# Optimization experiments

Hardware: AMD Instinct MI355X
Metric: run time of the kernel (lower is better)

## Reference

```python
import jax, jax.numpy as jnp
import numpy as np

DIM = 1024
NUM_HEADS = 16
HEAD_DIM = DIM // NUM_HEADS
SCALE = 1.0 / float(np.sqrt(HEAD_DIM))


def setup_inputs() -> dict:
    key = jax.random.key(0)
    ks = jax.random.split(key, 5)
    B, S = 2, 2048
    x = jax.random.normal(ks[0], (B, S, DIM), dtype=jnp.float32)
    qkv_w = jax.random.normal(ks[1], (3 * DIM, DIM), dtype=jnp.float32) * (1.0 / np.sqrt(DIM))
    qkv_b = jax.random.normal(ks[2], (3 * DIM,), dtype=jnp.float32) * 0.02
    proj_w = jax.random.normal(ks[3], (DIM, DIM), dtype=jnp.float32) * (1.0 / np.sqrt(DIM))
    proj_b = jax.random.normal(ks[4], (DIM,), dtype=jnp.float32) * 0.02
    return {"x": x, "qkv_w": qkv_w, "qkv_b": qkv_b, "proj_w": proj_w, "proj_b": proj_b}


def reference(x, qkv_w, qkv_b, proj_w, proj_b):
    B, S, _ = x.shape
    # qkv projection: (B,S,3*DIM) -> (3, B, H, S, Dh)
    qkv = x @ qkv_w.T + qkv_b
    qkv = qkv.reshape(B, S, 3, NUM_HEADS, HEAD_DIM).transpose(2, 0, 3, 1, 4)
    q, k, v = qkv[0], qkv[1], qkv[2]
    # scaled dot-product attention (full score matrix, as in the original)
    scores = jnp.einsum('bhqd,bhkd->bhqk', q, k) * SCALE
    attn = jax.nn.softmax(scores, axis=-1)
    out = jnp.einsum('bhqk,bhkd->bhqd', attn, v)  # (B,H,S,Dh)
    out = out.transpose(0, 2, 1, 3).reshape(B, S, DIM)
    return out @ proj_w.T + proj_b
```

## Files before the change

### kernel.cpp

```cpp
#include <hip/hip_runtime.h>

#define DIM_ 1024
#define NH_ 16
#define HD_ 64
#define B_ 2
#define S_ 2048
#define M_ (B_ * S_)
#define NQKV_ (3 * DIM_)

typedef __attribute__((ext_vector_type(8))) __bf16 bf16x8;
typedef __attribute__((ext_vector_type(4))) __bf16 bf16x4;
typedef __attribute__((ext_vector_type(4))) float f32x4;

__device__ __forceinline__ void gl_lds16(const void* g, void* l) {
  __builtin_amdgcn_global_load_lds(
      (__attribute__((address_space(1))) void*)const_cast<void*>(g),
      (__attribute__((address_space(3))) void*)l, 16, 0, 0);
}

#define N4_X 1048576
#define N4_W1 786432
#define N4_W2 262144
__global__ __launch_bounds__(256) void cast_all(const float* __restrict__ x,
                                                const float* __restrict__ w1,
                                                const float* __restrict__ w2,
                                                __bf16* __restrict__ xb,
                                                __bf16* __restrict__ w1b,
                                                __bf16* __restrict__ w2b) {
  int i = blockIdx.x * 256 + threadIdx.x;
  const int stride = gridDim.x * 256;
  for (; i < N4_X + N4_W1 + N4_W2; i += stride) {
    const float4* src;
    bf16x4* dst;
    int j;
    if (i < N4_X) { src = (const float4*)x; dst = (bf16x4*)xb; j = i; }
    else if (i < N4_X + N4_W1) { src = (const float4*)w1; dst = (bf16x4*)w1b; j = i - N4_X; }
    else { src = (const float4*)w2; dst = (bf16x4*)w2b; j = i - (N4_X + N4_W1); }
    float4 v = src[j];
    bf16x4 o;
    o[0] = (__bf16)v.x; o[1] = (__bf16)v.y; o[2] = (__bf16)v.z; o[3] = (__bf16)v.w;
    dst[j] = o;
  }
}

template <int MODE, int BM>
__global__ __launch_bounds__(512, 4) void gemm_bt(const __bf16* __restrict__ A,
                                                  const __bf16* __restrict__ Bw,
                                                  const float* __restrict__ bias,
                                                  __bf16* __restrict__ Qp, __bf16* __restrict__ Kp,
                                                  __bf16* __restrict__ Vt,
                                                  float* __restrict__ Cout) {
  constexpr int KD = 1024;
  constexpr int BN = 128;
  constexpr int MT = BM / 64;
  constexpr int NC = (BM + BN) / 64;
  __shared__ __bf16 As[BM * 64];
  __shared__ __bf16 Bs[BN * 64];
  const int tid = threadIdx.x;
  const int lane = tid & 63;
  const int wave = tid >> 6;
  const int quad = lane >> 4;
  const int r16 = lane & 15;
  const int wm = wave >> 1;
  const int wn = wave & 1;
  const int m0 = blockIdx.y * BM;
  const int n0 = blockIdx.x * BN;

  const f32x4 fz = {0.f, 0.f, 0.f, 0.f};
  f32x4 acc[MT][4];
#pragma unroll
  for (int i = 0; i < MT; ++i)
#pragma unroll
    for (int j = 0; j < 4; ++j) acc[i][j] = fz;

  const __bf16* gp[NC];
  __bf16* lp[NC];
#pragma unroll
  for (int i = 0; i < NC; ++i) {
    const int c = tid + i * 512;
    if (c < BM * 8) {
      const int r = c >> 3, cc = c & 7;
      gp[i] = A + (size_t)(m0 + r) * KD + ((cc ^ (r & 7)) * 8);
      lp[i] = &As[c * 8];
    } else {
      const int c2 = c - BM * 8;
      const int r = c2 >> 3, cc = c2 & 7;
      gp[i] = Bw + (size_t)(n0 + r) * KD + ((cc ^ (r & 7)) * 8);
      lp[i] = &Bs[c2 * 8];
    }
  }

  for (int kt = 0; kt < KD / 64; ++kt) {
    __syncthreads();
#pragma unroll
    for (int i = 0; i < NC; ++i) { gl_lds16(gp[i], lp[i]); gp[i] += 64; }
    __syncthreads();

#pragma unroll
    for (int sub = 0; sub < 2; ++sub) {
      const int ch = ((sub * 4 + quad) ^ (r16 & 7)) * 8;
      bf16x8 af[MT], bfr[4];
#pragma unroll
      for (int mt = 0; mt < MT; ++mt)
        af[mt] = *(const bf16x8*)&As[(wm * MT * 16 + mt * 16 + r16) * 64 + ch];
#pragma unroll
      for (int nt = 0; nt < 4; ++nt)
        bfr[nt] = *(const bf16x8*)&Bs[(wn * 64 + nt * 16 + r16) * 64 + ch];
#pragma unroll
      for (int mt = 0; mt < MT; ++mt)
#pragma unroll
        for (int nt = 0; nt < 4; ++nt)
          acc[mt][nt] =
              __builtin_amdgcn_mfma_f32_16x16x32_bf16(af[mt], bfr[nt], acc[mt][nt], 0, 0, 0);
    }
  }

  if (MODE == 0) {
#pragma unroll
    for (int nt = 0; nt < 4; ++nt) {
      const int n = n0 + wn * 64 + nt * 16 + r16;
      const int sel = n >> 10;
      const int h = (n >> 6) & 15;
      const int dh = n & 63;
      const float bs = bias[n];
      if (sel == 2) {
#pragma unroll
        for (int mt = 0; mt < MT; ++mt) {
          const int m = m0 + wm * MT * 16 + mt * 16 + quad * 4;
          const int b = m >> 11;
          const int s = m & 2047;
          const int slot = (s & ~31) | (((s >> 2) & 3) << 3) | (((s >> 4) & 1) << 2);
          bf16x4 ov;
#pragma unroll
          for (int r = 0; r < 4; ++r) ov[r] = (__bf16)(acc[mt][nt][r] + bs);
          *(bf16x4*)&Vt[((size_t)((b * NH_ + h) * HD_ + dh)) * S_ + slot] = ov;
        }
      } else {
        __bf16* dst = (sel == 0) ? Qp : Kp;
        const float mul = (sel == 0) ? 0.18033688011112042f : 1.0f;
#pragma unroll
        for (int mt = 0; mt < MT; ++mt) {
#pragma unroll
          for (int r = 0; r < 4; ++r) {
            const int m = m0 + wm * MT * 16 + mt * 16 + quad * 4 + r;
            const int b = m >> 11;
            const int s = m & 2047;
            dst[((size_t)((b * NH_ + h) * S_ + s)) * HD_ + dh] =
                (__bf16)((acc[mt][nt][r] + bs) * mul);
          }
        }
      }
    }
  } else {
#pragma unroll
    for (int nt = 0; nt < 4; ++nt) {
      const int n = n0 + wn * 64 + nt * 16 + r16;
      const float bs = bias[n];
#pragma unroll
      for (int mt = 0; mt < MT; ++mt) {
#pragma unroll
        for (int r = 0; r < 4; ++r) {
          const int m = m0 + wm * MT * 16 + mt * 16 + quad * 4 + r;
          Cout[(size_t)m * DIM_ + n] = acc[mt][nt][r] + bs;
        }
      }
    }
  }
}

__global__ __launch_bounds__(512, 4) void attn(const __bf16* __restrict__ Qp,
                                               const __bf16* __restrict__ Kp,
                                               const __bf16* __restrict__ Vtp,
                                               __bf16* __restrict__ ctx) {
  __shared__ alignas(16) char smem[65536];
  __bf16* KsB = (__bf16*)smem;
  __bf16* VsB = (__bf16*)(smem + 32768);
  const int tid = threadIdx.x;
  const int lane = tid & 63;
  const int wave = tid >> 6;
  const int quad = lane >> 4;
  const int r16 = lane & 15;
  const int kh = wave >> 2;
  const int ww = wave & 3;

  const int w = blockIdx.y * 16 + blockIdx.x;
  const int bh = (w & 7) + (((w >> 3) >> 4) << 3);
  const int q0 = ((w >> 3) & 15) * 128;

  const __bf16* qg0 = Qp + ((size_t)bh * S_ + (q0 + ww * 32 + r16)) * HD_;
  const __bf16* qg1 = qg0 + 16 * HD_;
  const bf16x8 qa0 = *(const bf16x8*)(qg0 + quad * 8);
  const bf16x8 qa1 = *(const bf16x8*)(qg0 + 32 + quad * 8);
  const bf16x8 qc0 = *(const bf16x8*)(qg1 + quad * 8);
  const bf16x8 qc1 = *(const bf16x8*)(qg1 + 32 + quad * 8);

  const f32x4 fz = {0.f, 0.f, 0.f, 0.f};
  f32x4 o0[4], o1[4];
#pragma unroll
  for (int d = 0; d < 4; ++d) { o0[d] = fz; o1[d] = fz; }
  float ls0 = 0.f, ls1 = 0.f;

  const __bf16* gk[2];
  const __bf16* gv[2];
  int lk[2], lv[2];
#pragma unroll
  for (int i = 0; i < 2; ++i) {
    const int c = tid + i * 512;
    const int half = c >> 9;
    const int r = (c >> 3) & 63;
    const int cc = c & 7;
    gk[i] = Kp + ((size_t)bh * S_ + half * 1024 + r) * HD_ + ((cc ^ (r & 7)) * 8);
    lk[i] = c * 8;
    gv[i] = Vtp + ((size_t)bh * HD_ + r) * S_ + half * 1024 + ((cc ^ (r & 7)) * 8);
    lv[i] = c * 8;
  }

#pragma unroll
  for (int i = 0; i < 2; ++i) {
    gl_lds16(gk[i], KsB + lk[i]); gk[i] += 64 * HD_;
    gl_lds16(gv[i], VsB + lv[i]); gv[i] += 64;
  }

  constexpr int NT = 1024 / 64;
  for (int kt = 0; kt < NT; ++kt) {
    const int cb = kt & 1;
    __syncthreads();
    if (kt + 1 < NT) {
#pragma unroll
      for (int i = 0; i < 2; ++i) {
        gl_lds16(gk[i], KsB + (cb ^ 1) * 8192 + lk[i]); gk[i] += 64 * HD_;
        gl_lds16(gv[i], VsB + (cb ^ 1) * 8192 + lv[i]); gv[i] += 64;
      }
    }

    const __bf16* Kt = KsB + cb * 8192 + kh * 4096;
    const __bf16* Vt2 = VsB + cb * 8192 + kh * 4096;

#pragma unroll
    for (int ks = 0; ks < 2; ++ks) {
      const int row0 = ks * 32 + r16;
      const int row1 = row0 + 16;
      const int xa = (quad ^ (r16 & 7)) * 8;
      const int xb = ((4 + quad) ^ (r16 & 7)) * 8;
      const bf16x8 k00 = *(const bf16x8*)&Kt[row0 * 64 + xa];
      const bf16x8 k01 = *(const bf16x8*)&Kt[row0 * 64 + xb];
      const bf16x8 k10 = *(const bf16x8*)&Kt[row1 * 64 + xa];
      const bf16x8 k11 = *(const bf16x8*)&Kt[row1 * 64 + xb];
      f32x4 t00 = fz, t01 = fz, t10 = fz, t11 = fz;
      t00 = __builtin_amdgcn_mfma_f32_16x16x32_bf16(k00, qa0, t00, 0, 0, 0);
      t00 = __builtin_amdgcn_mfma_f32_16x16x32_bf16(k01, qa1, t00, 0, 0, 0);
      t01 = __builtin_amdgcn_mfma_f32_16x16x32_bf16(k10, qa0, t01, 0, 0, 0);
      t01 = __builtin_amdgcn_mfma_f32_16x16x32_bf16(k11, qa1, t01, 0, 0, 0);
      t10 = __builtin_amdgcn_mfma_f32_16x16x32_bf16(k00, qc0, t10, 0, 0, 0);
      t10 = __builtin_amdgcn_mfma_f32_16x16x32_bf16(k01, qc1, t10, 0, 0, 0);
      t11 = __builtin_amdgcn_mfma_f32_16x16x32_bf16(k10, qc0, t11, 0, 0, 0);
      t11 = __builtin_amdgcn_mfma_f32_16x16x32_bf16(k11, qc1, t11, 0, 0, 0);

      bf16x8 pf0, pf1;
#pragma unroll
      for (int r = 0; r < 4; ++r) {
        const float p00 = __builtin_amdgcn_exp2f(t00[r]);
        const float p01 = __builtin_amdgcn_exp2f(t01[r]);
        const float p10 = __builtin_amdgcn_exp2f(t10[r]);
        const float p11 = __builtin_amdgcn_exp2f(t11[r]);
        ls0 += p00 + p01;
        ls1 += p10 + p11;
        pf0[r] = (__bf16)p00; pf0[4 + r] = (__bf16)p01;
        pf1[r] = (__bf16)p10; pf1[4 + r] = (__bf16)p11;
      }

#pragma unroll
      for (int dt = 0; dt < 4; ++dt) {
        const int row = dt * 16 + r16;
        const bf16x8 va = *(const bf16x8*)&Vt2[row * 64 + (((4 * ks + quad) ^ (r16 & 7)) * 8)];
        o0[dt] = __builtin_amdgcn_mfma_f32_16x16x32_bf16(va, pf0, o0[dt], 0, 0, 0);
        o1[dt] = __builtin_amdgcn_mfma_f32_16x16x32_bf16(va, pf1, o1[dt], 0, 0, 0);
      }
    }
  }

  ls0 += __shfl_xor(ls0, 16);
  ls0 += __shfl_xor(ls0, 32);
  ls1 += __shfl_xor(ls1, 16);
  ls1 += __shfl_xor(ls1, 32);

  __syncthreads();
  float* xfer = (float*)smem;
  float* p = xfer + (ww * 64 + lane) * 36;
  if (kh) {
    *(f32x4*)(p + 0) = o0[0];  *(f32x4*)(p + 4) = o0[1];
    *(f32x4*)(p + 8) = o0[2];  *(f32x4*)(p + 12) = o0[3];
    *(f32x4*)(p + 16) = o1[0]; *(f32x4*)(p + 20) = o1[1];
    *(f32x4*)(p + 24) = o1[2]; *(f32x4*)(p + 28) = o1[3];
    p[32] = ls0; p[33] = ls1;
  }
  __syncthreads();
  if (!kh) {
    o0[0] += *(const f32x4*)(p + 0);  o0[1] += *(const f32x4*)(p + 4);
    o0[2] += *(const f32x4*)(p + 8);  o0[3] += *(const f32x4*)(p + 12);
    o1[0] += *(const f32x4*)(p + 16); o1[1] += *(const f32x4*)(p + 20);
    o1[2] += *(const f32x4*)(p + 24); o1[3] += *(const f32x4*)(p + 28);
    ls0 += p[32]; ls1 += p[33];
    const float inv0 = 1.0f / ls0;
    const float inv1 = 1.0f / ls1;
    const int b = bh >> 4, h = bh & 15;
    const int s0 = q0 + ww * 32 + r16;
    const int s1 = s0 + 16;
#pragma unroll
    for (int dt = 0; dt < 4; ++dt) {
      bf16x4 ov0, ov1;
#pragma unroll
      for (int r = 0; r < 4; ++r) {
        ov0[r] = (__bf16)(o0[dt][r] * inv0);
        ov1[r] = (__bf16)(o1[dt][r] * inv1);
      }
      *(bf16x4*)&ctx[((size_t)(b * S_ + s0)) * DIM_ + h * 64 + dt * 16 + quad * 4] = ov0;
      *(bf16x4*)&ctx[((size_t)(b * S_ + s1)) * DIM_ + h * 64 + dt * 16 + quad * 4] = ov1;
    }
  }
}

extern "C" void kernel_launch(void* const* d_in, const int* in_sizes, int n_in, void* d_out,
                              int out_size, void* d_ws, size_t ws_size, hipStream_t stream) {
  const float* x = (const float*)d_in[0];
  const float* qkv_w = (const float*)d_in[1];
  const float* qkv_b = (const float*)d_in[2];
  const float* proj_w = (const float*)d_in[3];
  const float* proj_b = (const float*)d_in[4];
  float* out = (float*)d_out;

  char* ws = (char*)d_ws;
  __bf16* Xb = (__bf16*)(ws);
  __bf16* Wb = (__bf16*)(ws + 8388608);
  __bf16* Pb = (__bf16*)(ws + 14680064);
  __bf16* Qp = (__bf16*)(ws + 16777216);
  __bf16* Kp = (__bf16*)(ws + 25165824);
  __bf16* Vt = (__bf16*)(ws + 33554432);
  __bf16* Cx = (__bf16*)(ws + 41943040);

  cast_all<<<2048, 256, 0, stream>>>(x, qkv_w, proj_w, Xb, Wb, Pb);
  gemm_bt<0, 128><<<dim3(NQKV_ / 128, M_ / 128), 512, 0, stream>>>(Xb, Wb, qkv_b, Qp, Kp, Vt,
                                                                   nullptr);
  attn<<<dim3(S_ / 128, 32), 512, 0, stream>>>(Qp, Kp, Vt, Cx);
  gemm_bt<1, 64><<<dim3(DIM_ / 128, M_ / 64), 512, 0, stream>>>(Cx, Pb, proj_b, nullptr, nullptr,
                                                                nullptr, out);
}
```

Before: 164.6 us.

## Halve attention block to 4 waves, each covering 64 query rows

The attention kernel now runs 256 threads per block instead of 512. Each wave handles 64 query rows (four 16-row groups) instead of 32, so every K and V fragment read from LDS is reused across four MFMA groups, and each thread issues twice as many async global-to-LDS loads. It also raises wave priority around the MFMA bursts with s_setprio. The cost is more accumulator registers per thread and fewer waves per block, with launch bounds changed to (256,2).

Measured after the change: 167.3 us. Within noise of the previous version (+1.6%).

```diff
diff --git a/kernel.cpp b/kernel.cpp
--- a/kernel.cpp
+++ b/kernel.cpp
@@ -168,7 +168,7 @@
   }
 }
 
-__global__ __launch_bounds__(512, 4) void attn(const __bf16* __restrict__ Qp,
+__global__ __launch_bounds__(256, 2) void attn(const __bf16* __restrict__ Qp,
                                                const __bf16* __restrict__ Kp,
                                                const __bf16* __restrict__ Vtp,
                                                __bf16* __restrict__ ctx) {
@@ -180,32 +180,35 @@
   const int wave = tid >> 6;
   const int quad = lane >> 4;
   const int r16 = lane & 15;
-  const int kh = wave >> 2;
-  const int ww = wave & 3;
+  const int kh = wave >> 1;
+  const int wq = wave & 1;
 
   const int w = blockIdx.y * 16 + blockIdx.x;
   const int bh = (w & 7) + (((w >> 3) >> 4) << 3);
   const int q0 = ((w >> 3) & 15) * 128;
 
-  const __bf16* qg0 = Qp + ((size_t)bh * S_ + (q0 + ww * 32 + r16)) * HD_;
-  const __bf16* qg1 = qg0 + 16 * HD_;
-  const bf16x8 qa0 = *(const bf16x8*)(qg0 + quad * 8);
-  const bf16x8 qa1 = *(const bf16x8*)(qg0 + 32 + quad * 8);
-  const bf16x8 qc0 = *(const bf16x8*)(qg1 + quad * 8);
-  const bf16x8 qc1 = *(const bf16x8*)(qg1 + 32 + quad * 8);
+  bf16x8 qf[4][2];
+#pragma unroll
+  for (int g = 0; g < 4; ++g) {
+    const __bf16* qg = Qp + ((size_t)bh * S_ + (q0 + wq * 64 + g * 16 + r16)) * HD_;
+    qf[g][0] = *(const bf16x8*)(qg + quad * 8);
+    qf[g][1] = *(const bf16x8*)(qg + 32 + quad * 8);
+  }
 
   const f32x4 fz = {0.f, 0.f, 0.f, 0.f};
-  f32x4 o0[4], o1[4];
-#pragma unroll
-  for (int d = 0; d < 4; ++d) { o0[d] = fz; o1[d] = fz; }
-  float ls0 = 0.f, ls1 = 0.f;
-
-  const __bf16* gk[2];
-  const __bf16* gv[2];
-  int lk[2], lv[2];
-#pragma unroll
-  for (int i = 0; i < 2; ++i) {
-    const int c = tid + i * 512;
+  f32x4 o[4][4];
+#pragma unroll
+  for (int g = 0; g < 4; ++g)
+#pragma unroll
+    for (int d = 0; d < 4; ++d) o[g][d] = fz;
+  float ls[4] = {0.f, 0.f, 0.f, 0.f};
+
+  const __bf16* gk[4];
+  const __bf16* gv[4];
+  int lk[4], lv[4];
+#pragma unroll
+  for (int i = 0; i < 4; ++i) {
+    const int c = tid + i * 256;
     const int half = c >> 9;
     const int r = (c >> 3) & 63;
     const int cc = c & 7;
@@ -216,7 +219,7 @@
   }
 
 #pragma unroll
-  for (int i = 0; i < 2; ++i) {
+  for (int i = 0; i < 4; ++i) {
     gl_lds16(gk[i], KsB + lk[i]); gk[i] += 64 * HD_;
     gl_lds16(gv[i], VsB + lv[i]); gv[i] += 64;
   }
@@ -227,7 +230,7 @@
     __syncthreads();
     if (kt + 1 < NT) {
 #pragma unroll
-      for (int i = 0; i < 2; ++i) {
+      for (int i = 0; i < 4; ++i) {
         gl_lds16(gk[i], KsB + (cb ^ 1) * 8192 + lk[i]); gk[i] += 64 * HD_;
         gl_lds16(gv[i], VsB + (cb ^ 1) * 8192 + lv[i]); gv[i] += 64;
       }
@@ -246,76 +249,81 @@
       const bf16x8 k01 = *(const bf16x8*)&Kt[row0 * 64 + xb];
       const bf16x8 k10 = *(const bf16x8*)&Kt[row1 * 64 + xa];
       const bf16x8 k11 = *(const bf16x8*)&Kt[row1 * 64 + xb];
-      f32x4 t00 = fz, t01 = fz, t10 = fz, t11 = fz;
-      t00 = __builtin_amdgcn_mfma_f32_16x16x32_bf16(k00, qa0, t00, 0, 0, 0);
-      t00 = __builtin_amdgcn_mfma_f32_16x16x32_bf16(k01, qa1, t00, 0, 0, 0);
-      t01 = __builtin_amdgcn_mfma_f32_16x16x32_bf16(k10, qa0, t01, 0, 0, 0);
-      t01 = __builtin_amdgcn_mfma_f32_16x16x32_bf16(k11, qa1, t01, 0, 0, 0);
-      t10 = __builtin_amdgcn_mfma_f32_16x16x32_bf16(k00, qc0, t10, 0, 0, 0);
-      t10 = __builtin_amdgcn_mfma_f32_16x16x32_bf16(k01, qc1, t10, 0, 0, 0);
-      t11 = __builtin_amdgcn_mfma_f32_16x16x32_bf16(k10, qc0, t11, 0, 0, 0);
-      t11 = __builtin_amdgcn_mfma_f32_16x16x32_bf16(k11, qc1, t11, 0, 0, 0);
-
-      bf16x8 pf0, pf1;
-#pragma unroll
-      for (int r = 0; r < 4; ++r) {
-        const float p00 = __builtin_amdgcn_exp2f(t00[r]);
-        const float p01 = __builtin_amdgcn_exp2f(t01[r]);
-        const float p10 = __builtin_amdgcn_exp2f(t10[r]);
-        const float p11 = __builtin_amdgcn_exp2f(t11[r]);
-        ls0 += p00 + p01;
-        ls1 += p10 + p11;
-        pf0[r] = (__bf16)p00; pf0[4 + r] = (__bf16)p01;
-        pf1[r] = (__bf16)p10; pf1[4 + r] = (__bf16)p11;
-      }
-
+      f32x4 t0[4], t1[4];
+      __builtin_amdgcn_s_setprio(1);
+#pragma unroll
+      for (int g = 0; g < 4; ++g) {
+        f32x4 a = fz, b = fz;
+        a = __builtin_amdgcn_mfma_f32_16x16x32_bf16(k00, qf[g][0], a, 0, 0, 0);
+        a = __builtin_amdgcn_mfma_f32_16x16x32_bf16(k01, qf[g][1], a, 0, 0, 0);
+        b = __builtin_amdgcn_mfma_f32_16x16x32_bf16(k10, qf[g][0], b, 0, 0, 0);
+        b = __builtin_amdgcn_mfma_f32_16x16x32_bf16(k11, qf[g][1], b, 0, 0, 0);
+        t0[g] = a;
+        t1[g] = b;
+      }
+      __builtin_amdgcn_s_setprio(0);
+
+      bf16x8 pf[4];
+#pragma unroll
+      for (int g = 0; g < 4; ++g)
+#pragma unroll
+        for (int r = 0; r < 4; ++r) {
+          const float p0 = __builtin_amdgcn_exp2f(t0[g][r]);
+          const float p1 = __builtin_amdgcn_exp2f(t1[g][r]);
+          ls[g] += p0 + p1;
+          pf[g][r] = (__bf16)p0;
+          pf[g][4 + r] = (__bf16)p1;
+        }
+
+      bf16x8 va[4];
 #pragma unroll
       for (int dt = 0; dt < 4; ++dt) {
         const int row = dt * 16 + r16;
-        const bf16x8 va = *(const bf16x8*)&Vt2[row * 64 + (((4 * ks + quad) ^ (r16 & 7)) * 8)];
-        o0[dt] = __builtin_amdgcn_mfma_f32_16x16x32_bf16(va, pf0, o0[dt], 0, 0, 0);
-        o1[dt] = __builtin_amdgcn_mfma_f32_16x16x32_bf16(va, pf1, o1[dt], 0, 0, 0);
-      }
-    }
-  }
-
-  ls0 += __shfl_xor(ls0, 16);
-  ls0 += __shfl_xor(ls0, 32);
-  ls1 += __shfl_xor(ls1, 16);
-  ls1 += __shfl_xor(ls1, 32);
+        va[dt] = *(const bf16x8*)&Vt2[row * 64 + (((4 * ks + quad) ^ (r16 & 7)) * 8)];
+      }
+      __builtin_amdgcn_s_setprio(1);
+#pragma unroll
+      for (int dt = 0; dt < 4; ++dt)
+#pragma unroll
+        for (int g = 0; g < 4; ++g)
+          o[g][dt] = __builtin_amdgcn_mfma_f32_16x16x32_bf16(va[dt], pf[g], o[g][dt], 0, 0, 0);
+      __builtin_amdgcn_s_setprio(0);
+    }
+  }
+
+#pragma unroll
+  for (int g = 0; g < 4; ++g) {
+    ls[g] += __shfl_xor(ls[g], 16);
+    ls[g] += __shfl_xor(ls[g], 32);
+  }
 
   __syncthreads();
   float* xfer = (float*)smem;
-  float* p = xfer + (ww * 64 + lane) * 36;
+  float* p = xfer + (wq * 64 + lane) * 76;
   if (kh) {
-    *(f32x4*)(p + 0) = o0[0];  *(f32x4*)(p + 4) = o0[1];
-    *(f32x4*)(p + 8) = o0[2];  *(f32x4*)(p + 12) = o0[3];
-    *(f32x4*)(p + 16) = o1[0]; *(f32x4*)(p + 20) = o1[1];
-    *(f32x4*)(p + 24) = o1[2]; *(f32x4*)(p + 28) = o1[3];
-    p[32] = ls0; p[33] = ls1;
+#pragma unroll
+    for (int g = 0; g < 4; ++g)
+#pragma unroll
+      for (int dt = 0; dt < 4; ++dt) *(f32x4*)(p + (g * 4 + dt) * 4) = o[g][dt];
+#pragma unroll
+    for (int g = 0; g < 4; ++g) p[64 + g] = ls[g];
   }
   __syncthreads();
   if (!kh) {
-    o0[0] += *(const f32x4*)(p + 0);  o0[1] += *(const f32x4*)(p + 4);
-    o0[2] += *(const f32x4*)(p + 8);  o0[3] += *(const f32x4*)(p + 12);
-    o1[0] += *(const f32x4*)(p + 16); o1[1] += *(const f32x4*)(p + 20);
-    o1[2] += *(const f32x4*)(p + 24); o1[3] += *(const f32x4*)(p + 28);
-    ls0 += p[32]; ls1 += p[33];
-    const float inv0 = 1.0f / ls0;
-    const float inv1 = 1.0f / ls1;
     const int b = bh >> 4, h = bh & 15;
-    const int s0 = q0 + ww * 32 + r16;
-    const int s1 = s0 + 16;
-#pragma unroll
-    for (int dt = 0; dt < 4; ++dt) {
-      bf16x4 ov0, ov1;
-#pragma unroll
-      for (int r = 0; r < 4; ++r) {
-        ov0[r] = (__bf16)(o0[dt][r] * inv0);
-        ov1[r] = (__bf16)(o1[dt][r] * inv1);
-      }
-      *(bf16x4*)&ctx[((size_t)(b * S_ + s0)) * DIM_ + h * 64 + dt * 16 + quad * 4] = ov0;
-      *(bf16x4*)&ctx[((size_t)(b * S_ + s1)) * DIM_ + h * 64 + dt * 16 + quad * 4] = ov1;
+#pragma unroll
+    for (int g = 0; g < 4; ++g) {
+#pragma unroll
+      for (int dt = 0; dt < 4; ++dt) o[g][dt] += *(const f32x4*)(p + (g * 4 + dt) * 4);
+      const float inv = 1.0f / (ls[g] + p[64 + g]);
+      const int s = q0 + wq * 64 + g * 16 + r16;
+#pragma unroll
+      for (int dt = 0; dt < 4; ++dt) {
+        bf16x4 ov;
+#pragma unroll
+        for (int r = 0; r < 4; ++r) ov[r] = (__bf16)(o[g][dt][r] * inv);
+        *(bf16x4*)&ctx[((size_t)(b * S_ + s)) * DIM_ + h * 64 + dt * 16 + quad * 4] = ov;
+      }
     }
   }
 }
@@ -341,7 +349,7 @@
   cast_all<<<2048, 256, 0, stream>>>(x, qkv_w, proj_w, Xb, Wb, Pb);
   gemm_bt<0, 128><<<dim3(NQKV_ / 128, M_ / 128), 512, 0, stream>>>(Xb, Wb, qkv_b, Qp, Kp, Vt,
                                                                    nullptr);
-  attn<<<dim3(S_ / 128, 32), 512, 0, stream>>>(Qp, Kp, Vt, Cx);
+  attn<<<dim3(S_ / 128, 32), 256, 0, stream>>>(Qp, Kp, Vt, Cx);
   gemm_bt<1, 64><<<dim3(DIM_ / 128, M_ / 64), 512, 0, stream>>>(Cx, Pb, proj_b, nullptr, nullptr,
                                                                 nullptr, out);
 }
```

## Double-buffer GEMM LDS tiles, remap workgroups across XCDs, enlarge GEMM tiles

Applied to the files above, without the earlier changes.

The bf16 GEMM kernel now keeps two LDS stages. Global-to-LDS loads for tile k+2 are issued while MFMAs run on tile k, gated by explicit vmcnt waits and raw barriers instead of two __syncthreads per iteration. Workgroup IDs are remapped so consecutive tiles land on the same XCD for better L2 reuse. MFMA sections get raised wave priority. Both GEMMs also use larger M tiles (256 for QKV, 128 for the projection) with launch bounds relaxed to two blocks per CU. The cost is more LDS per block and fewer resident blocks, so occupancy drops.

After: 173.7 us. 1.06x slower.

```diff
diff --git a/kernel.cpp b/kernel.cpp
--- a/kernel.cpp
+++ b/kernel.cpp
@@ -44,7 +44,7 @@
 }
 
 template <int MODE, int BM>
-__global__ __launch_bounds__(512, 4) void gemm_bt(const __bf16* __restrict__ A,
+__global__ __launch_bounds__(512, 2) void gemm_bt(const __bf16* __restrict__ A,
                                                   const __bf16* __restrict__ Bw,
                                                   const float* __restrict__ bias,
                                                   __bf16* __restrict__ Qp, __bf16* __restrict__ Kp,
@@ -54,8 +54,8 @@
   constexpr int BN = 128;
   constexpr int MT = BM / 64;
   constexpr int NC = (BM + BN) / 64;
-  __shared__ __bf16 As[BM * 64];
-  __shared__ __bf16 Bs[BN * 64];
+  constexpr int NKT = KD / 64;
+  __shared__ __bf16 Tl[2][(BM + BN) * 64];
   const int tid = threadIdx.x;
   const int lane = tid & 63;
   const int wave = tid >> 6;
@@ -63,8 +63,13 @@
   const int r16 = lane & 15;
   const int wm = wave >> 1;
   const int wn = wave & 1;
-  const int m0 = blockIdx.y * BM;
-  const int n0 = blockIdx.x * BN;
+
+  const int gx = gridDim.x;
+  const int nwg = gx * gridDim.y;
+  const int w0 = blockIdx.y * gx + blockIdx.x;
+  const int wid = (w0 & 7) * (nwg >> 3) + (w0 >> 3);
+  const int m0 = (wid / gx) * BM;
+  const int n0 = (wid % gx) * BN;
 
   const f32x4 fz = {0.f, 0.f, 0.f, 0.f};
   f32x4 acc[MT][4];
@@ -74,45 +79,66 @@
     for (int j = 0; j < 4; ++j) acc[i][j] = fz;
 
   const __bf16* gp[NC];
-  __bf16* lp[NC];
+  int lofs[NC];
 #pragma unroll
   for (int i = 0; i < NC; ++i) {
     const int c = tid + i * 512;
+    lofs[i] = c * 8;
     if (c < BM * 8) {
       const int r = c >> 3, cc = c & 7;
       gp[i] = A + (size_t)(m0 + r) * KD + ((cc ^ (r & 7)) * 8);
-      lp[i] = &As[c * 8];
     } else {
       const int c2 = c - BM * 8;
       const int r = c2 >> 3, cc = c2 & 7;
       gp[i] = Bw + (size_t)(n0 + r) * KD + ((cc ^ (r & 7)) * 8);
-      lp[i] = &Bs[c2 * 8];
-    }
-  }
-
-  for (int kt = 0; kt < KD / 64; ++kt) {
-    __syncthreads();
-#pragma unroll
-    for (int i = 0; i < NC; ++i) { gl_lds16(gp[i], lp[i]); gp[i] += 64; }
-    __syncthreads();
-
+    }
+  }
+
+  auto stage = [&](int buf) {
+#pragma unroll
+    for (int i = 0; i < NC; ++i) {
+      gl_lds16(gp[i], &Tl[buf][lofs[i]]);
+      gp[i] += 64;
+    }
+  };
+
+  stage(0);
+  stage(1);
+
+  for (int kt = 0; kt < NKT; ++kt) {
+    const int cb = kt & 1;
+    if (kt < NKT - 1) {
+      if constexpr (NC == 6) asm volatile("s_waitcnt vmcnt(6)" ::: "memory");
+      else asm volatile("s_waitcnt vmcnt(4)" ::: "memory");
+    } else {
+      asm volatile("s_waitcnt vmcnt(0)" ::: "memory");
+    }
+    __builtin_amdgcn_s_barrier();
+
+    const __bf16* Asb = Tl[cb];
+    const __bf16* Bsb = Tl[cb] + BM * 64;
 #pragma unroll
     for (int sub = 0; sub < 2; ++sub) {
       const int ch = ((sub * 4 + quad) ^ (r16 & 7)) * 8;
       bf16x8 af[MT], bfr[4];
 #pragma unroll
       for (int mt = 0; mt < MT; ++mt)
-        af[mt] = *(const bf16x8*)&As[(wm * MT * 16 + mt * 16 + r16) * 64 + ch];
+        af[mt] = *(const bf16x8*)&Asb[(wm * MT * 16 + mt * 16 + r16) * 64 + ch];
 #pragma unroll
       for (int nt = 0; nt < 4; ++nt)
-        bfr[nt] = *(const bf16x8*)&Bs[(wn * 64 + nt * 16 + r16) * 64 + ch];
+        bfr[nt] = *(const bf16x8*)&Bsb[(wn * 64 + nt * 16 + r16) * 64 + ch];
+      __builtin_amdgcn_s_setprio(1);
 #pragma unroll
       for (int mt = 0; mt < MT; ++mt)
 #pragma unroll
         for (int nt = 0; nt < 4; ++nt)
           acc[mt][nt] =
               __builtin_amdgcn_mfma_f32_16x16x32_bf16(af[mt], bfr[nt], acc[mt][nt], 0, 0, 0);
-    }
+      __builtin_amdgcn_s_setprio(0);
+    }
+    asm volatile("" ::: "memory");
+    __builtin_amdgcn_s_barrier();
+    if (kt + 2 < NKT) stage(cb);
   }
 
   if (MODE == 0) {
@@ -339,9 +365,9 @@
   __bf16* Cx = (__bf16*)(ws + 41943040);
 
   cast_all<<<2048, 256, 0, stream>>>(x, qkv_w, proj_w, Xb, Wb, Pb);
-  gemm_bt<0, 128><<<dim3(NQKV_ / 128, M_ / 128), 512, 0, stream>>>(Xb, Wb, qkv_b, Qp, Kp, Vt,
+  gemm_bt<0, 256><<<dim3(NQKV_ / 128, M_ / 256), 512, 0, stream>>>(Xb, Wb, qkv_b, Qp, Kp, Vt,
                                                                    nullptr);
   attn<<<dim3(S_ / 128, 32), 512, 0, stream>>>(Qp, Kp, Vt, Cx);
-  gemm_bt<1, 64><<<dim3(DIM_ / 128, M_ / 64), 512, 0, stream>>>(Cx, Pb, proj_b, nullptr, nullptr,
-                                                                nullptr, out);
-}
+  gemm_bt<1, 128><<<dim3(DIM_ / 128, M_ / 128), 512, 0, stream>>>(Cx, Pb, proj_b, nullptr,
+                                                                  nullptr, nullptr, out);
+}
```

## Load V fragments directly from global memory instead of staging through LDS

Applied to the files above, without the earlier changes.

The attention kernel stops staging V tiles through shared memory. Each lane now reads its V fragment straight from global memory into registers every step. This cuts LDS use from 64KB to 40KB and raises the occupancy hint from 4 to 6 blocks per CU, aiming to remove the V LDS traffic and fit more waves. The cost is uncached, latency-exposed global loads that are no longer software-pipelined, plus more register pressure under the tighter launch bound.

Result: slower. 468.2 us (+184.5%).

```diff
diff --git a/kernel.cpp b/kernel.cpp
--- a/kernel.cpp
+++ b/kernel.cpp
@@ -168,13 +168,12 @@
   }
 }
 
-__global__ __launch_bounds__(512, 4) void attn(const __bf16* __restrict__ Qp,
+__global__ __launch_bounds__(512, 6) void attn(const __bf16* __restrict__ Qp,
                                                const __bf16* __restrict__ Kp,
                                                const __bf16* __restrict__ Vtp,
                                                __bf16* __restrict__ ctx) {
-  __shared__ alignas(16) char smem[65536];
+  __shared__ alignas(16) char smem[40960];
   __bf16* KsB = (__bf16*)smem;
-  __bf16* VsB = (__bf16*)(smem + 32768);
   const int tid = threadIdx.x;
   const int lane = tid & 63;
   const int wave = tid >> 6;
@@ -200,9 +199,13 @@
   for (int d = 0; d < 4; ++d) { o0[d] = fz; o1[d] = fz; }
   float ls0 = 0.f, ls1 = 0.f;
 
+  const __bf16* vp[4];
+#pragma unroll
+  for (int dt = 0; dt < 4; ++dt)
+    vp[dt] = Vtp + ((size_t)(bh * 64 + dt * 16 + r16)) * S_ + kh * 1024 + quad * 8;
+
   const __bf16* gk[2];
-  const __bf16* gv[2];
-  int lk[2], lv[2];
+  int lk[2];
 #pragma unroll
   for (int i = 0; i < 2; ++i) {
     const int c = tid + i * 512;
@@ -211,15 +214,10 @@
     const int cc = c & 7;
     gk[i] = Kp + ((size_t)bh * S_ + half * 1024 + r) * HD_ + ((cc ^ (r & 7)) * 8);
     lk[i] = c * 8;
-    gv[i] = Vtp + ((size_t)bh * HD_ + r) * S_ + half * 1024 + ((cc ^ (r & 7)) * 8);
-    lv[i] = c * 8;
-  }
-
-#pragma unroll
-  for (int i = 0; i < 2; ++i) {
-    gl_lds16(gk[i], KsB + lk[i]); gk[i] += 64 * HD_;
-    gl_lds16(gv[i], VsB + lv[i]); gv[i] += 64;
-  }
+  }
+
+#pragma unroll
+  for (int i = 0; i < 2; ++i) { gl_lds16(gk[i], KsB + lk[i]); gk[i] += 64 * HD_; }
 
   constexpr int NT = 1024 / 64;
   for (int kt = 0; kt < NT; ++kt) {
@@ -227,17 +225,18 @@
     __syncthreads();
     if (kt + 1 < NT) {
 #pragma unroll
-      for (int i = 0; i < 2; ++i) {
-        gl_lds16(gk[i], KsB + (cb ^ 1) * 8192 + lk[i]); gk[i] += 64 * HD_;
-        gl_lds16(gv[i], VsB + (cb ^ 1) * 8192 + lv[i]); gv[i] += 64;
-      }
+      for (int i = 0; i < 2; ++i) { gl_lds16(gk[i], KsB + (cb ^ 1) * 8192 + lk[i]); gk[i] += 64 * HD_; }
     }
 
     const __bf16* Kt = KsB + cb * 8192 + kh * 4096;
-    const __bf16* Vt2 = VsB + cb * 8192 + kh * 4096;
 
 #pragma unroll
     for (int ks = 0; ks < 2; ++ks) {
+      bf16x8 va[4];
+#pragma unroll
+      for (int dt = 0; dt < 4; ++dt)
+        va[dt] = *(const bf16x8*)(vp[dt] + kt * 64 + ks * 32);
+
       const int row0 = ks * 32 + r16;
       const int row1 = row0 + 16;
       const int xa = (quad ^ (r16 & 7)) * 8;
@@ -271,10 +270,8 @@
 
 #pragma unroll
       for (int dt = 0; dt < 4; ++dt) {
-        const int row = dt * 16 + r16;
-        const bf16x8 va = *(const bf16x8*)&Vt2[row * 64 + (((4 * ks + quad) ^ (r16 & 7)) * 8)];
-        o0[dt] = __builtin_amdgcn_mfma_f32_16x16x32_bf16(va, pf0, o0[dt], 0, 0, 0);
-        o1[dt] = __builtin_amdgcn_mfma_f32_16x16x32_bf16(va, pf1, o1[dt], 0, 0, 0);
+        o0[dt] = __builtin_amdgcn_mfma_f32_16x16x32_bf16(va[dt], pf0, o0[dt], 0, 0, 0);
+        o1[dt] = __builtin_amdgcn_mfma_f32_16x16x32_bf16(va[dt], pf1, o1[dt], 0, 0, 0);
       }
     }
   }
```
